# Kernel optimization log

Hardware: AMD Instinct MI355X
Metric: run time of the kernel (lower is better)

The kernel has to match this reference:

```python
import jax, jax.numpy as jnp
import numpy as np

N_NODES = 100000
N_EDGES = 600000
N_FEAT = 128
HIDDEN = 128
N_CLASSES = 40  # output dim = num_classes + 1 = 41


def setup_inputs() -> dict:
    key = jax.random.key(0)
    k = jax.random.split(key, 6)
    x = jax.random.normal(k[0], (N_NODES, N_FEAT), dtype=jnp.float32)
    edge_index = jax.random.randint(k[1], (2, N_EDGES), 0, N_NODES, dtype=jnp.int64)
    # GCNConv params (Glorot-ish scale)
    W1 = jax.random.normal(k[2], (N_FEAT, HIDDEN), dtype=jnp.float32) / np.sqrt(N_FEAT)
    b1 = jnp.zeros((HIDDEN,), dtype=jnp.float32)
    W2 = jax.random.normal(k[3], (HIDDEN, N_CLASSES + 1), dtype=jnp.float32) / np.sqrt(HIDDEN)
    b2 = jnp.zeros((N_CLASSES + 1,), dtype=jnp.float32)
    return {"x": x, "W1": W1, "b1": b1, "W2": W2, "b2": b2, "edge_index": edge_index}


def _gcn_layer(x, W, b, src, dst, norm, n):
    # linear transform then normalized scatter-add aggregation (PyG GCNConv)
    h = x @ W                                  # [N, out]
    msg = h[src] * norm[:, None]               # gather + per-edge normalization
    out = jax.ops.segment_sum(msg, dst, num_segments=n)
    return out + b


def reference(x, W1, b1, W2, b2, edge_index):
    n = x.shape[0]
    # add self-loops
    loops = jnp.arange(n, dtype=edge_index.dtype)
    src = jnp.concatenate([edge_index[0], loops])
    dst = jnp.concatenate([edge_index[1], loops])
    # symmetric degree normalization: D^{-1/2} A_hat D^{-1/2}
    deg = jax.ops.segment_sum(jnp.ones_like(dst, dtype=x.dtype), dst, num_segments=n)
    dinv = jnp.where(deg > 0, jax.lax.rsqrt(deg), 0.0)
    norm = dinv[src] * dinv[dst]               # [E + N]
    h = _gcn_layer(x, W1, b1, src, dst, norm, n)
    h = jax.nn.relu(h)
    # dropout is identity in eval mode
    h = _gcn_layer(h, W2, b2, src, dst, norm, n)
    return jax.nn.log_softmax(h, axis=1)
```

## Files before the change

### kernel.cpp

```cpp
#include <hip/hip_runtime.h>
#include <math.h>

#define N_NODES 100000
#define N_EDGES 600000
#define NC 41
#define NT (N_NODES / 16)
#define NB ((N_NODES + 255) / 256)
#define G1B 1024
#define CNTB ((N_EDGES + 255) / 256)

typedef __attribute__((ext_vector_type(8))) short bf16x8;
typedef __attribute__((ext_vector_type(8))) unsigned short u16x8;
typedef __attribute__((ext_vector_type(4))) float f32x4;

static __device__ __forceinline__ unsigned short f2b(float f) {
    unsigned u = __float_as_uint(f);
    unsigned r = ((u >> 16) & 1u) + 0x7fffu;
    return (unsigned short)((u + r) >> 16);
}
static __device__ __forceinline__ float b2f(unsigned short s) {
    return __uint_as_float(((unsigned)s) << 16);
}
static __device__ __forceinline__ u16x8 zero8() {
    u16x8 z;
#pragma unroll
    for (int i = 0; i < 8; ++i) z[i] = 0;
    return z;
}

__global__ __launch_bounds__(256) void k_pre(const float* __restrict__ x,
                                             const float* __restrict__ W,
                                             unsigned short* __restrict__ h,
                                             const int* __restrict__ dst,
                                             int* __restrict__ cnt) {
    __shared__ unsigned short Wt[128 * 132];
    int tid = threadIdx.x;
    for (int i = tid; i < 128 * 128; i += 256) {
        int k = i >> 7, n = i & 127;
        Wt[n * 132 + k] = f2b(W[i]);
    }
    __syncthreads();

    int l = tid & 63, w = tid >> 6;
    int lr = l & 15, g = l >> 4;

    bf16x8 bf[2][4];
#pragma unroll
    for (int c = 0; c < 2; ++c) {
        int n = (w * 2 + c) * 16 + lr;
#pragma unroll
        for (int kt = 0; kt < 4; ++kt) {
            const unsigned short* p = &Wt[n * 132 + kt * 32 + g * 4];
            short4 lo = *(const short4*)p;
            short4 hi = *(const short4*)(p + 16);
            bf16x8 f;
            f[0] = lo.x; f[1] = lo.y; f[2] = lo.z; f[3] = lo.w;
            f[4] = hi.x; f[5] = hi.y; f[6] = hi.z; f[7] = hi.w;
            bf[c][kt] = f;
        }
    }

    for (int t = blockIdx.x; t < NT; t += G1B) {
        int row = t * 16 + lr;
        const float4* xr = (const float4*)(x + (size_t)row * 128);
        f32x4 acc0 = {0.f, 0.f, 0.f, 0.f};
        f32x4 acc1 = {0.f, 0.f, 0.f, 0.f};
#pragma unroll
        for (int kt = 0; kt < 4; ++kt) {
            float4 alo = xr[kt * 8 + g];
            float4 ahi = xr[kt * 8 + 4 + g];
            bf16x8 a;
            a[0] = (short)f2b(alo.x); a[1] = (short)f2b(alo.y);
            a[2] = (short)f2b(alo.z); a[3] = (short)f2b(alo.w);
            a[4] = (short)f2b(ahi.x); a[5] = (short)f2b(ahi.y);
            a[6] = (short)f2b(ahi.z); a[7] = (short)f2b(ahi.w);
            acc0 = __builtin_amdgcn_mfma_f32_16x16x32_bf16(a, bf[0][kt], acc0, 0, 0, 0);
            acc1 = __builtin_amdgcn_mfma_f32_16x16x32_bf16(a, bf[1][kt], acc1, 0, 0, 0);
        }
        int c0 = (w * 2) * 16 + lr;
        int rbase = t * 16 + g * 4;
#pragma unroll
        for (int i = 0; i < 4; ++i) {
            h[(size_t)(rbase + i) * 128 + c0] = f2b(acc0[i]);
            h[(size_t)(rbase + i) * 128 + c0 + 16] = f2b(acc1[i]);
        }
    }

    for (int e = blockIdx.x * 256 + tid; e < N_EDGES; e += G1B * 256)
        atomicAdd(&cnt[dst[e]], 1);
}

__global__ __launch_bounds__(256) void k_blocksum(const int* __restrict__ cnt,
                                                  int* __restrict__ bsum,
                                                  float* __restrict__ dinv, int n) {
    __shared__ int tmp[256];
    int t = threadIdx.x, gid = blockIdx.x * 256 + t;
    int v = (gid < n) ? cnt[gid] : 0;
    if (gid < n) dinv[gid] = rsqrtf((float)(v + 1));
    tmp[t] = v;
    __syncthreads();
    for (int d = 128; d; d >>= 1) {
        if (t < d) tmp[t] += tmp[t + d];
        __syncthreads();
    }
    if (t == 0) bsum[blockIdx.x] = tmp[0];
}

__global__ __launch_bounds__(512) void k_scanb(int* __restrict__ bsum, int nb) {
    __shared__ int tmp[512];
    int t = threadIdx.x;
    int v = (t < nb) ? bsum[t] : 0;
    tmp[t] = v;
    __syncthreads();
    for (int d = 1; d < 512; d <<= 1) {
        int u = (t >= d) ? tmp[t - d] : 0;
        __syncthreads();
        tmp[t] += u;
        __syncthreads();
    }
    if (t < nb) bsum[t] = tmp[t] - v;
}

__global__ __launch_bounds__(256) void k_scanfinal(int* __restrict__ cnt,
                                                   const int* __restrict__ bsum,
                                                   int* __restrict__ off, int n) {
    __shared__ int tmp[256];
    int t = threadIdx.x, gid = blockIdx.x * 256 + t;
    int v = (gid < n) ? cnt[gid] : 0;
    tmp[t] = v;
    __syncthreads();
    for (int d = 1; d < 256; d <<= 1) {
        int u = (t >= d) ? tmp[t - d] : 0;
        __syncthreads();
        tmp[t] += u;
        __syncthreads();
    }
    int ex = tmp[t] - v + bsum[blockIdx.x];
    if (gid < n) {
        off[gid] = ex;
        cnt[gid] = ex;
    }
    if (gid == 0) off[n] = N_EDGES;
}

__global__ void k_scatter(const int* __restrict__ src, const int* __restrict__ dst,
                          const float* __restrict__ dinv,
                          int* __restrict__ cursor, int2* __restrict__ eidx, int E) {
    int e = blockIdx.x * blockDim.x + threadIdx.x;
    if (e >= E) return;
    int s = src[e];
    int d = dst[e];
    float ds = dinv[s];
    int pos = atomicAdd(&cursor[d], 1);
    eidx[pos] = make_int2(s, __float_as_int(ds));
}

__global__ __launch_bounds__(256, 8) void k_agg1mm(const unsigned short* __restrict__ h,
                                                   const float* __restrict__ W2,
                                                   const float* __restrict__ dinv,
                                                   const float* __restrict__ b1,
                                                   const int* __restrict__ off,
                                                   const int2* __restrict__ eidx,
                                                   unsigned short* __restrict__ h2) {
    __shared__ unsigned short Wt[48 * 132];
    __shared__ unsigned short rows[16 * 136];
    int tid = threadIdx.x;
    for (int i = tid; i < 128 * 48; i += 256) {
        int k = i / 48, n = i % 48;
        Wt[n * 132 + k] = f2b((n < NC) ? W2[k * NC + n] : 0.f);
    }
    __syncthreads();

    int l = tid & 63, w = tid >> 6;
    int j = l & 15;
    int nloc = w * 4 + (l >> 4);
    int lr = l & 15, g = l >> 4;

    for (int t = blockIdx.x; t < NT; t += gridDim.x) {
        int node = t * 16 + nloc;
        float di = dinv[node];
        float acc[8];
        {
            u16x8 v = *(const u16x8*)(h + (size_t)node * 128 + j * 8);
#pragma unroll
            for (int i = 0; i < 8; ++i) acc[i] = b2f(v[i]) * di;
        }
        int beg = off[node], end = off[node + 1];
        int e = beg;
        int2 p0 = (e < end) ? eidx[e] : make_int2(-1, 0);
        int2 p1 = (e + 1 < end) ? eidx[e + 1] : make_int2(-1, 0);
        u16x8 r0 = zero8(), r1 = zero8();
        if (p0.x >= 0) r0 = *(const u16x8*)(h + (size_t)p0.x * 128 + j * 8);
        if (p1.x >= 0) r1 = *(const u16x8*)(h + (size_t)p1.x * 128 + j * 8);
        while (p0.x >= 0) {
            int2 p2 = (e + 2 < end) ? eidx[e + 2] : make_int2(-1, 0);
            u16x8 r2 = zero8();
            if (p2.x >= 0) r2 = *(const u16x8*)(h + (size_t)p2.x * 128 + j * 8);
            float nm = __int_as_float(p0.y);
#pragma unroll
            for (int i = 0; i < 8; ++i) acc[i] = fmaf(b2f(r0[i]), nm, acc[i]);
            p0 = p1; p1 = p2; r0 = r1; r1 = r2; ++e;
        }
        float4 blo = ((const float4*)b1)[j * 2];
        float4 bhi = ((const float4*)b1)[j * 2 + 1];
        u16x8 o;
        o[0] = f2b(fmaxf(acc[0] * di + blo.x, 0.f));
        o[1] = f2b(fmaxf(acc[1] * di + blo.y, 0.f));
        o[2] = f2b(fmaxf(acc[2] * di + blo.z, 0.f));
        o[3] = f2b(fmaxf(acc[3] * di + blo.w, 0.f));
        o[4] = f2b(fmaxf(acc[4] * di + bhi.x, 0.f));
        o[5] = f2b(fmaxf(acc[5] * di + bhi.y, 0.f));
        o[6] = f2b(fmaxf(acc[6] * di + bhi.z, 0.f));
        o[7] = f2b(fmaxf(acc[7] * di + bhi.w, 0.f));
        *(u16x8*)&rows[nloc * 136 + j * 8] = o;
        __syncthreads();

        if (w < 3) {
            f32x4 a0 = {0.f, 0.f, 0.f, 0.f};
#pragma unroll
            for (int kt = 0; kt < 4; ++kt) {
                const unsigned short* pa = &rows[lr * 136 + kt * 32 + g * 4];
                short4 alo = *(const short4*)pa;
                short4 ahi = *(const short4*)(pa + 16);
                bf16x8 a;
                a[0] = alo.x; a[1] = alo.y; a[2] = alo.z; a[3] = alo.w;
                a[4] = ahi.x; a[5] = ahi.y; a[6] = ahi.z; a[7] = ahi.w;
                const unsigned short* pb = &Wt[(w * 16 + lr) * 132 + kt * 32 + g * 4];
                short4 wlo = *(const short4*)pb;
                short4 whi = *(const short4*)(pb + 16);
                bf16x8 bb;
                bb[0] = wlo.x; bb[1] = wlo.y; bb[2] = wlo.z; bb[3] = wlo.w;
                bb[4] = whi.x; bb[5] = whi.y; bb[6] = whi.z; bb[7] = whi.w;
                a0 = __builtin_amdgcn_mfma_f32_16x16x32_bf16(a, bb, a0, 0, 0, 0);
            }
            int rbase = t * 16 + g * 4;
#pragma unroll
            for (int i = 0; i < 4; ++i) {
                float dv = dinv[rbase + i];
                h2[(size_t)(rbase + i) * 64 + w * 16 + lr] = f2b(a0[i] * dv);
            }
        }
        __syncthreads();
    }
}

__global__ __launch_bounds__(256, 8) void k_gather2(const unsigned short* __restrict__ h2,
                                                    float* __restrict__ out,
                                                    const int* __restrict__ off,
                                                    const int2* __restrict__ eidx,
                                                    const float* __restrict__ dinv,
                                                    const float* __restrict__ b2) {
    __shared__ float so[8 * NC + 8];
    int tid = threadIdx.x;
    int nloc = tid >> 5;
    int node = blockIdx.x * 8 + nloc;
    int l = tid & 31;
    int g = l >> 3, j = l & 7;
    bool act = (j < 6);
    float di = dinv[node];
    float acc[8];
#pragma unroll
    for (int i = 0; i < 8; ++i) acc[i] = 0.f;
    if (g == 0 && act) {
        u16x8 v = *(const u16x8*)(h2 + (size_t)node * 64 + j * 8);
#pragma unroll
        for (int i = 0; i < 8; ++i) acc[i] = b2f(v[i]);
    }
    int beg = off[node], end = off[node + 1];
    int e = beg + g;
    int s0 = (e < end) ? eidx[e].x : -1;
    int s1 = (e + 4 < end) ? eidx[e + 4].x : -1;
    u16x8 r0 = zero8(), r1 = zero8();
    if (s0 >= 0 && act) r0 = *(const u16x8*)(h2 + (size_t)s0 * 64 + j * 8);
    if (s1 >= 0 && act) r1 = *(const u16x8*)(h2 + (size_t)s1 * 64 + j * 8);
    while (s0 >= 0) {
        int s2 = (e + 8 < end) ? eidx[e + 8].x : -1;
        u16x8 r2 = zero8();
        if (s2 >= 0 && act) r2 = *(const u16x8*)(h2 + (size_t)s2 * 64 + j * 8);
#pragma unroll
        for (int i = 0; i < 8; ++i) acc[i] += b2f(r0[i]);
        s0 = s1; s1 = s2; r0 = r1; r1 = r2; e += 4;
    }
#pragma unroll
    for (int i = 0; i < 8; ++i) acc[i] += __shfl_xor(acc[i], 8);
#pragma unroll
    for (int i = 0; i < 8; ++i) acc[i] += __shfl_xor(acc[i], 16);
    int c0 = j * 8;
    float vv[8];
#pragma unroll
    for (int i = 0; i < 8; ++i)
        vv[i] = (act && c0 + i < NC) ? acc[i] * di + b2[c0 + i] : -INFINITY;
    float m = vv[0];
#pragma unroll
    for (int i = 1; i < 8; ++i) m = fmaxf(m, vv[i]);
#pragma unroll
    for (int o = 4; o; o >>= 1) m = fmaxf(m, __shfl_xor(m, o));
    float sm = 0.f;
#pragma unroll
    for (int i = 0; i < 8; ++i) sm += (act && c0 + i < NC) ? expf(vv[i] - m) : 0.f;
#pragma unroll
    for (int o = 4; o; o >>= 1) sm += __shfl_xor(sm, o);
    float lg = logf(sm);
    if (g == 0 && act) {
#pragma unroll
        for (int i = 0; i < 8; ++i) {
            int c = c0 + i;
            if (c < NC) so[nloc * NC + c] = vv[i] - m - lg;
        }
    }
    __syncthreads();
    float4* ob = (float4*)(out + (size_t)blockIdx.x * (8 * NC));
    const float4* sb = (const float4*)so;
    if (tid < 2 * NC) ob[tid] = sb[tid];
}

extern "C" void kernel_launch(void* const* d_in, const int* in_sizes, int n_in,
                              void* d_out, int out_size, void* d_ws, size_t ws_size,
                              hipStream_t stream) {
    const float* x  = (const float*)d_in[0];
    const float* W1 = (const float*)d_in[1];
    const float* b1 = (const float*)d_in[2];
    const float* W2 = (const float*)d_in[3];
    const float* b2 = (const float*)d_in[4];
    const int*   ei = (const int*)d_in[5];
    const int* src = ei;
    const int* dst = ei + N_EDGES;
    float* out = (float*)d_out;

    char* ws = (char*)d_ws;
    int*   cnt  = (int*)ws;
    int*   off  = cnt + N_NODES + 32;
    int*   bsum = off + N_NODES + 32;
    float* dinv = (float*)(bsum + 512);
    int2*  eidx = (int2*)(dinv + N_NODES + 32);
    unsigned short* h1 = (unsigned short*)(ws + (8u << 20));
    unsigned short* h2 = h1 + (size_t)N_NODES * 128;

    hipMemsetAsync(cnt, 0, N_NODES * sizeof(int), stream);
    k_pre<<<G1B, 256, 0, stream>>>(x, W1, h1, dst, cnt);
    k_blocksum<<<NB, 256, 0, stream>>>(cnt, bsum, dinv, N_NODES);
    k_scanb<<<1, 512, 0, stream>>>(bsum, NB);
    k_scanfinal<<<NB, 256, 0, stream>>>(cnt, bsum, off, N_NODES);
    k_scatter<<<CNTB, 256, 0, stream>>>(src, dst, dinv, cnt, eidx, N_EDGES);

    k_agg1mm<<<2048, 256, 0, stream>>>(h1, W2, dinv, b1, off, eidx, h2);

    k_gather2<<<N_NODES / 8, 256, 0, stream>>>(h2, out, off, eidx, dinv, b2);
}
```

Measured before the change: 178.2 us.

## Aggregate raw features before W1 and fuse both GEMMs into one kernel

Layer 1 is reordered to A_hat·(X·W1). The old path computed X·W1 in the pre-pass and then aggregated. Now the pre-pass only converts x to bf16 and counts degrees, a separate kernel aggregates the bf16 features into R, and a new 512-thread kernel runs R·W1 + b1, ReLU and ·W2 back to back through shared memory. Because the input and hidden widths are both 128, the gather traffic is unchanged. The intent is to split the latency-bound gather from the MFMA work, so that each kernel gets a better launch and occupancy configuration. The cost is an extra full pass writing and reading R and xb (bf16 N×128), one more kernel launch, and a different bf16 rounding order.

```diff
diff --git a/kernel.cpp b/kernel.cpp
--- a/kernel.cpp
+++ b/kernel.cpp
@@ -4,9 +4,8 @@
 #define N_NODES 100000
 #define N_EDGES 600000
 #define NC 41
-#define NT (N_NODES / 16)
 #define NB ((N_NODES + 255) / 256)
-#define G1B 1024
+#define PREB 2048
 #define CNTB ((N_EDGES + 255) / 256)
 
 typedef __attribute__((ext_vector_type(8))) short bf16x8;
@@ -28,65 +27,21 @@
     return z;
 }
 
-__global__ __launch_bounds__(256) void k_pre(const float* __restrict__ x,
-                                             const float* __restrict__ W,
-                                             unsigned short* __restrict__ h,
-                                             const int* __restrict__ dst,
-                                             int* __restrict__ cnt) {
-    __shared__ unsigned short Wt[128 * 132];
-    int tid = threadIdx.x;
-    for (int i = tid; i < 128 * 128; i += 256) {
-        int k = i >> 7, n = i & 127;
-        Wt[n * 132 + k] = f2b(W[i]);
-    }
-    __syncthreads();
-
-    int l = tid & 63, w = tid >> 6;
-    int lr = l & 15, g = l >> 4;
-
-    bf16x8 bf[2][4];
-#pragma unroll
-    for (int c = 0; c < 2; ++c) {
-        int n = (w * 2 + c) * 16 + lr;
-#pragma unroll
-        for (int kt = 0; kt < 4; ++kt) {
-            const unsigned short* p = &Wt[n * 132 + kt * 32 + g * 4];
-            short4 lo = *(const short4*)p;
-            short4 hi = *(const short4*)(p + 16);
-            bf16x8 f;
-            f[0] = lo.x; f[1] = lo.y; f[2] = lo.z; f[3] = lo.w;
-            f[4] = hi.x; f[5] = hi.y; f[6] = hi.z; f[7] = hi.w;
-            bf[c][kt] = f;
-        }
-    }
-
-    for (int t = blockIdx.x; t < NT; t += G1B) {
-        int row = t * 16 + lr;
-        const float4* xr = (const float4*)(x + (size_t)row * 128);
-        f32x4 acc0 = {0.f, 0.f, 0.f, 0.f};
-        f32x4 acc1 = {0.f, 0.f, 0.f, 0.f};
-#pragma unroll
-        for (int kt = 0; kt < 4; ++kt) {
-            float4 alo = xr[kt * 8 + g];
-            float4 ahi = xr[kt * 8 + 4 + g];
-            bf16x8 a;
-            a[0] = (short)f2b(alo.x); a[1] = (short)f2b(alo.y);
-            a[2] = (short)f2b(alo.z); a[3] = (short)f2b(alo.w);
-            a[4] = (short)f2b(ahi.x); a[5] = (short)f2b(ahi.y);
-            a[6] = (short)f2b(ahi.z); a[7] = (short)f2b(ahi.w);
-            acc0 = __builtin_amdgcn_mfma_f32_16x16x32_bf16(a, bf[0][kt], acc0, 0, 0, 0);
-            acc1 = __builtin_amdgcn_mfma_f32_16x16x32_bf16(a, bf[1][kt], acc1, 0, 0, 0);
-        }
-        int c0 = (w * 2) * 16 + lr;
-        int rbase = t * 16 + g * 4;
-#pragma unroll
-        for (int i = 0; i < 4; ++i) {
-            h[(size_t)(rbase + i) * 128 + c0] = f2b(acc0[i]);
-            h[(size_t)(rbase + i) * 128 + c0 + 16] = f2b(acc1[i]);
-        }
-    }
-
-    for (int e = blockIdx.x * 256 + tid; e < N_EDGES; e += G1B * 256)
+__global__ __launch_bounds__(256) void k_prep(const float* __restrict__ x,
+                                              unsigned short* __restrict__ xb,
+                                              const int* __restrict__ dst,
+                                              int* __restrict__ cnt) {
+    int tid = blockIdx.x * 256 + threadIdx.x;
+    const int nthr = PREB * 256;
+    for (int i = tid; i < N_NODES * 128 / 8; i += nthr) {
+        float4 lo = ((const float4*)x)[i * 2];
+        float4 hi = ((const float4*)x)[i * 2 + 1];
+        u16x8 o;
+        o[0] = f2b(lo.x); o[1] = f2b(lo.y); o[2] = f2b(lo.z); o[3] = f2b(lo.w);
+        o[4] = f2b(hi.x); o[5] = f2b(hi.y); o[6] = f2b(hi.z); o[7] = f2b(hi.w);
+        ((u16x8*)xb)[i] = o;
+    }
+    for (int e = tid; e < N_EDGES; e += nthr)
         atomicAdd(&cnt[dst[e]], 1);
 }
 
@@ -155,89 +110,145 @@
     eidx[pos] = make_int2(s, __float_as_int(ds));
 }
 
-__global__ __launch_bounds__(256, 8) void k_agg1mm(const unsigned short* __restrict__ h,
-                                                   const float* __restrict__ W2,
-                                                   const float* __restrict__ dinv,
-                                                   const float* __restrict__ b1,
-                                                   const int* __restrict__ off,
-                                                   const int2* __restrict__ eidx,
-                                                   unsigned short* __restrict__ h2) {
-    __shared__ unsigned short Wt[48 * 132];
-    __shared__ unsigned short rows[16 * 136];
+__global__ __launch_bounds__(256, 8) void k_aggx(const unsigned short* __restrict__ xb,
+                                                 const float* __restrict__ dinv,
+                                                 const int* __restrict__ off,
+                                                 const int2* __restrict__ eidx,
+                                                 unsigned short* __restrict__ R) {
     int tid = threadIdx.x;
-    for (int i = tid; i < 128 * 48; i += 256) {
+    int node = blockIdx.x * 16 + (tid >> 4);
+    int j = tid & 15;
+    float di = dinv[node];
+    float acc[8];
+    {
+        u16x8 v = *(const u16x8*)(xb + (size_t)node * 128 + j * 8);
+#pragma unroll
+        for (int i = 0; i < 8; ++i) acc[i] = b2f(v[i]) * di;
+    }
+    int beg = off[node], end = off[node + 1];
+    int e = beg;
+    int2 p0 = (e < end) ? eidx[e] : make_int2(-1, 0);
+    int2 p1 = (e + 1 < end) ? eidx[e + 1] : make_int2(-1, 0);
+    u16x8 r0 = zero8(), r1 = zero8();
+    if (p0.x >= 0) r0 = *(const u16x8*)(xb + (size_t)p0.x * 128 + j * 8);
+    if (p1.x >= 0) r1 = *(const u16x8*)(xb + (size_t)p1.x * 128 + j * 8);
+    while (p0.x >= 0) {
+        int2 p2 = (e + 2 < end) ? eidx[e + 2] : make_int2(-1, 0);
+        u16x8 r2 = zero8();
+        if (p2.x >= 0) r2 = *(const u16x8*)(xb + (size_t)p2.x * 128 + j * 8);
+        float nm = __int_as_float(p0.y);
+#pragma unroll
+        for (int i = 0; i < 8; ++i) acc[i] = fmaf(b2f(r0[i]), nm, acc[i]);
+        p0 = p1; p1 = p2; r0 = r1; r1 = r2; ++e;
+    }
+    u16x8 o;
+#pragma unroll
+    for (int i = 0; i < 8; ++i) o[i] = f2b(acc[i] * di);
+    *(u16x8*)(R + (size_t)node * 128 + j * 8) = o;
+}
+
+__global__ __launch_bounds__(512) void k_mm(const unsigned short* __restrict__ R,
+                                            const float* __restrict__ W1,
+                                            const float* __restrict__ b1,
+                                            const float* __restrict__ W2,
+                                            const float* __restrict__ dinv,
+                                            unsigned short* __restrict__ h2) {
+    __shared__ unsigned short Wt1[128 * 132];
+    __shared__ unsigned short Wt2[48 * 132];
+    __shared__ unsigned short rows[32 * 136];
+    int tid = threadIdx.x;
+    for (int i = tid; i < 128 * 128; i += 512) {
+        int k = i >> 7, n = i & 127;
+        Wt1[n * 132 + k] = f2b(W1[i]);
+    }
+    for (int i = tid; i < 128 * 48; i += 512) {
         int k = i / 48, n = i % 48;
-        Wt[n * 132 + k] = f2b((n < NC) ? W2[k * NC + n] : 0.f);
+        Wt2[n * 132 + k] = f2b((n < NC) ? W2[k * NC + n] : 0.f);
     }
     __syncthreads();
 
     int l = tid & 63, w = tid >> 6;
-    int j = l & 15;
-    int nloc = w * 4 + (l >> 4);
     int lr = l & 15, g = l >> 4;
-
-    for (int t = blockIdx.x; t < NT; t += gridDim.x) {
-        int node = t * 16 + nloc;
-        float di = dinv[node];
-        float acc[8];
-        {
-            u16x8 v = *(const u16x8*)(h + (size_t)node * 128 + j * 8);
-#pragma unroll
-            for (int i = 0; i < 8; ++i) acc[i] = b2f(v[i]) * di;
-        }
-        int beg = off[node], end = off[node + 1];
-        int e = beg;
-        int2 p0 = (e < end) ? eidx[e] : make_int2(-1, 0);
-        int2 p1 = (e + 1 < end) ? eidx[e + 1] : make_int2(-1, 0);
-        u16x8 r0 = zero8(), r1 = zero8();
-        if (p0.x >= 0) r0 = *(const u16x8*)(h + (size_t)p0.x * 128 + j * 8);
-        if (p1.x >= 0) r1 = *(const u16x8*)(h + (size_t)p1.x * 128 + j * 8);
-        while (p0.x >= 0) {
-            int2 p2 = (e + 2 < end) ? eidx[e + 2] : make_int2(-1, 0);
-            u16x8 r2 = zero8();
-            if (p2.x >= 0) r2 = *(const u16x8*)(h + (size_t)p2.x * 128 + j * 8);
-            float nm = __int_as_float(p0.y);
-#pragma unroll
-            for (int i = 0; i < 8; ++i) acc[i] = fmaf(b2f(r0[i]), nm, acc[i]);
-            p0 = p1; p1 = p2; r0 = r1; r1 = r2; ++e;
-        }
-        float4 blo = ((const float4*)b1)[j * 2];
-        float4 bhi = ((const float4*)b1)[j * 2 + 1];
-        u16x8 o;
-        o[0] = f2b(fmaxf(acc[0] * di + blo.x, 0.f));
-        o[1] = f2b(fmaxf(acc[1] * di + blo.y, 0.f));
-        o[2] = f2b(fmaxf(acc[2] * di + blo.z, 0.f));
-        o[3] = f2b(fmaxf(acc[3] * di + blo.w, 0.f));
-        o[4] = f2b(fmaxf(acc[4] * di + bhi.x, 0.f));
-        o[5] = f2b(fmaxf(acc[5] * di + bhi.y, 0.f));
-        o[6] = f2b(fmaxf(acc[6] * di + bhi.z, 0.f));
-        o[7] = f2b(fmaxf(acc[7] * di + bhi.w, 0.f));
-        *(u16x8*)&rows[nloc * 136 + j * 8] = o;
-        __syncthreads();
-
-        if (w < 3) {
-            f32x4 a0 = {0.f, 0.f, 0.f, 0.f};
+    int rh = w >> 2;
+    int cg = w & 3;
+    int rh2 = w / 3, ct = w % 3;
+
+    bf16x8 f1[2][4];
+#pragma unroll
+    for (int c = 0; c < 2; ++c) {
+        int n = (cg * 2 + c) * 16 + lr;
+#pragma unroll
+        for (int kt = 0; kt < 4; ++kt) {
+            const unsigned short* p = &Wt1[n * 132 + kt * 32 + g * 4];
+            short4 lo = *(const short4*)p;
+            short4 hi = *(const short4*)(p + 16);
+            bf16x8 f;
+            f[0] = lo.x; f[1] = lo.y; f[2] = lo.z; f[3] = lo.w;
+            f[4] = hi.x; f[5] = hi.y; f[6] = hi.z; f[7] = hi.w;
+            f1[c][kt] = f;
+        }
+    }
+    bf16x8 f2[4];
+    if (w < 6) {
+#pragma unroll
+        for (int kt = 0; kt < 4; ++kt) {
+            const unsigned short* p = &Wt2[(ct * 16 + lr) * 132 + kt * 32 + g * 4];
+            short4 lo = *(const short4*)p;
+            short4 hi = *(const short4*)(p + 16);
+            bf16x8 f;
+            f[0] = lo.x; f[1] = lo.y; f[2] = lo.z; f[3] = lo.w;
+            f[4] = hi.x; f[5] = hi.y; f[6] = hi.z; f[7] = hi.w;
+            f2[kt] = f;
+        }
+    }
+    float bia0 = b1[(cg * 2) * 16 + lr];
+    float bia1 = b1[(cg * 2 + 1) * 16 + lr];
+
+    int srow = tid >> 4, scol = tid & 15;
+    for (int t = blockIdx.x; t < N_NODES / 32; t += gridDim.x) {
+        *(u16x8*)&rows[srow * 136 + scol * 8] =
+            *(const u16x8*)(R + ((size_t)t * 32 + srow) * 128 + scol * 8);
+        __syncthreads();
+
+        f32x4 a0 = {0.f, 0.f, 0.f, 0.f};
+        f32x4 a1 = {0.f, 0.f, 0.f, 0.f};
+#pragma unroll
+        for (int kt = 0; kt < 4; ++kt) {
+            const unsigned short* pa = &rows[(rh * 16 + lr) * 136 + kt * 32 + g * 4];
+            short4 alo = *(const short4*)pa;
+            short4 ahi = *(const short4*)(pa + 16);
+            bf16x8 a;
+            a[0] = alo.x; a[1] = alo.y; a[2] = alo.z; a[3] = alo.w;
+            a[4] = ahi.x; a[5] = ahi.y; a[6] = ahi.z; a[7] = ahi.w;
+            a0 = __builtin_amdgcn_mfma_f32_16x16x32_bf16(a, f1[0][kt], a0, 0, 0, 0);
+            a1 = __builtin_amdgcn_mfma_f32_16x16x32_bf16(a, f1[1][kt], a1, 0, 0, 0);
+        }
+        __syncthreads();
+
+#pragma unroll
+        for (int i = 0; i < 4; ++i) {
+            int row = rh * 16 + g * 4 + i;
+            rows[row * 136 + (cg * 2) * 16 + lr]     = f2b(fmaxf(a0[i] + bia0, 0.f));
+            rows[row * 136 + (cg * 2 + 1) * 16 + lr] = f2b(fmaxf(a1[i] + bia1, 0.f));
+        }
+        __syncthreads();
+
+        if (w < 6) {
+            f32x4 c0 = {0.f, 0.f, 0.f, 0.f};
 #pragma unroll
             for (int kt = 0; kt < 4; ++kt) {
-                const unsigned short* pa = &rows[lr * 136 + kt * 32 + g * 4];
+                const unsigned short* pa = &rows[(rh2 * 16 + lr) * 136 + kt * 32 + g * 4];
                 short4 alo = *(const short4*)pa;
                 short4 ahi = *(const short4*)(pa + 16);
                 bf16x8 a;
                 a[0] = alo.x; a[1] = alo.y; a[2] = alo.z; a[3] = alo.w;
                 a[4] = ahi.x; a[5] = ahi.y; a[6] = ahi.z; a[7] = ahi.w;
-                const unsigned short* pb = &Wt[(w * 16 + lr) * 132 + kt * 32 + g * 4];
-                short4 wlo = *(const short4*)pb;
-                short4 whi = *(const short4*)(pb + 16);
-                bf16x8 bb;
-                bb[0] = wlo.x; bb[1] = wlo.y; bb[2] = wlo.z; bb[3] = wlo.w;
-                bb[4] = whi.x; bb[5] = whi.y; bb[6] = whi.z; bb[7] = whi.w;
-                a0 = __builtin_amdgcn_mfma_f32_16x16x32_bf16(a, bb, a0, 0, 0, 0);
+                c0 = __builtin_amdgcn_mfma_f32_16x16x32_bf16(a, f2[kt], c0, 0, 0, 0);
             }
-            int rbase = t * 16 + g * 4;
 #pragma unroll
             for (int i = 0; i < 4; ++i) {
-                float dv = dinv[rbase + i];
-                h2[(size_t)(rbase + i) * 64 + w * 16 + lr] = f2b(a0[i] * dv);
+                int row = t * 32 + rh2 * 16 + g * 4 + i;
+                h2[(size_t)row * 64 + ct * 16 + lr] = f2b(c0[i] * dinv[row]);
             }
         }
         __syncthreads();
@@ -333,17 +344,19 @@
     int*   bsum = off + N_NODES + 32;
     float* dinv = (float*)(bsum + 512);
     int2*  eidx = (int2*)(dinv + N_NODES + 32);
-    unsigned short* h1 = (unsigned short*)(ws + (8u << 20));
-    unsigned short* h2 = h1 + (size_t)N_NODES * 128;
+    unsigned short* xb = (unsigned short*)(ws + (8u << 20));
+    unsigned short* R  = xb + (size_t)N_NODES * 128;
+    unsigned short* h2 = R + (size_t)N_NODES * 128;
 
     hipMemsetAsync(cnt, 0, N_NODES * sizeof(int), stream);
-    k_pre<<<G1B, 256, 0, stream>>>(x, W1, h1, dst, cnt);
+    k_prep<<<PREB, 256, 0, stream>>>(x, xb, dst, cnt);
     k_blocksum<<<NB, 256, 0, stream>>>(cnt, bsum, dinv, N_NODES);
     k_scanb<<<1, 512, 0, stream>>>(bsum, NB);
     k_scanfinal<<<NB, 256, 0, stream>>>(cnt, bsum, off, N_NODES);
     k_scatter<<<CNTB, 256, 0, stream>>>(src, dst, dinv, cnt, eidx, N_EDGES);
 
-    k_agg1mm<<<2048, 256, 0, stream>>>(h1, W2, dinv, b1, off, eidx, h2);
+    k_aggx<<<N_NODES / 16, 256, 0, stream>>>(xb, dinv, off, eidx, R);
+    k_mm<<<1024, 512, 0, stream>>>(R, W1, b1, W2, dinv, h2);
 
     k_gather2<<<N_NODES / 8, 256, 0, stream>>>(h2, out, off, eidx, dinv, b2);
 }
```

After: 186.6 us. 4.7% more time.
